# Kernel optimization log

Hardware: AMD Instinct MI355X
Metric: run time of the kernel (lower is better)

Reference implementation:

```python
import jax, jax.numpy as jnp
import numpy as np

SIZE = 8192
DIM = 256
N = 32768
BETA = 0.25
DECAY = 0.99
EPS = 1e-5


def setup_inputs() -> dict:
    key = jax.random.key(0)
    kz, ke = jax.random.split(key)
    z = jax.random.normal(kz, (N, DIM), dtype=jnp.float32)
    # init = randn * 0.1, ema_embed_sum initialized as a clone of embeddings
    embeddings = jax.random.normal(ke, (SIZE, DIM), dtype=jnp.float32) * 0.1
    ema_embed_sum = embeddings
    ema_cluster_size = jnp.zeros((SIZE,), dtype=jnp.float32)
    usage_counter = jnp.zeros((SIZE,), dtype=jnp.int64)
    return {
        "z": z,
        "embeddings": embeddings,
        "ema_cluster_size": ema_cluster_size,
        "ema_embed_sum": ema_embed_sum,
        "usage_counter": usage_counter,
    }


def reference(z, embeddings, ema_cluster_size, ema_embed_sum, usage_counter):
    # Squared euclidean distances; argmin is identical to cdist argmin.
    z2 = jnp.sum(z * z, axis=-1, keepdims=True)              # [N, 1]
    e2 = jnp.sum(embeddings * embeddings, axis=-1)           # [K]
    d2 = z2 - 2.0 * jnp.matmul(z, embeddings.T) + e2         # [N, K]
    indices = jnp.argmin(d2, axis=-1)                         # [N]

    quantized = embeddings[indices]                           # [N, D] gather

    # usage_counter: vectorized equivalent of the per-index python loop
    counts_f = jax.ops.segment_sum(
        jnp.ones((z.shape[0],), dtype=jnp.float32), indices, num_segments=SIZE
    )                                                         # [K] == onehot.sum(0)
    new_usage = usage_counter + counts_f.astype(usage_counter.dtype)

    sg = jax.lax.stop_gradient
    commit_loss = BETA * jnp.mean((z - sg(quantized)) ** 2)
    codebook_loss = jnp.mean((quantized - sg(z)) ** 2)
    loss = commit_loss + codebook_loss

    # EMA update (training mode), all under no-grad semantics
    embed_sum = jax.ops.segment_sum(z, indices, num_segments=SIZE)  # onehot.T @ z
    new_cluster_size = DECAY * ema_cluster_size + (1.0 - DECAY) * counts_f
    new_embed_sum = DECAY * ema_embed_sum + (1.0 - DECAY) * embed_sum
    n = jnp.sum(new_cluster_size)
    cluster = (new_cluster_size + EPS) / (n + SIZE * EPS) * n
    new_embeddings = new_embed_sum / cluster[:, None]

    # straight-through estimator
    quantized_st = z + sg(quantized - z)
    return (indices, quantized_st, loss, new_embeddings, new_cluster_size,
            new_embed_sum, new_usage)
```

## Files before the change

### kernel.cpp

```cpp
#include <hip/hip_runtime.h>

#define NZ 32768
#define KE 8192
#define DD 256
#define NCHUNK 4
#define CH (KE / NCHUNK)
#define NSLICE (NCHUNK * 4)
#define ITERS ((CH / 128) * 8)
#define THR_GAP 0.05f
#define BIASF 128.0f

typedef __attribute__((ext_vector_type(8))) _Float16 f16x8;
typedef __attribute__((ext_vector_type(4))) float f32x4;
typedef unsigned int uint32;


__device__ __forceinline__ float wave_reduce_sum(float v) {
#pragma unroll
  for (int m = 32; m >= 1; m >>= 1) v += __shfl_xor(v, m, 64);
  return v;
}

__global__ void prep_kernel(const float* __restrict__ emb, unsigned short* __restrict__ e_dst,
                            float* __restrict__ e_sq, const float* __restrict__ z,
                            unsigned short* __restrict__ z_dst,
                            const float* __restrict__ ema_cs, float* __restrict__ sema_out,
                            float* __restrict__ o_loss) {
  const int gb = blockIdx.x;
  if (gb < KE / 4) {
    const int row = gb * 4 + (threadIdx.x >> 6);
    const int lane = threadIdx.x & 63;
    const float4 v = *reinterpret_cast<const float4*>(emb + (size_t)row * DD + lane * 4);
    alignas(8) _Float16 hv[4] = {(_Float16)v.x, (_Float16)v.y, (_Float16)v.z, (_Float16)v.w};
    *reinterpret_cast<uint2*>(e_dst + (size_t)row * DD + lane * 4) =
        *reinterpret_cast<const uint2*>(hv);
    float s = (v.x * v.x + v.y * v.y) + (v.z * v.z + v.w * v.w);
    s = wave_reduce_sum(s);
    if (lane == 0) e_sq[row] = s;
  } else if (gb < (KE / 4) + (NZ / 4)) {
    const int row = (gb - KE / 4) * 4 + (threadIdx.x >> 6);
    const int lane = threadIdx.x & 63;
    const float4 v = *reinterpret_cast<const float4*>(z + (size_t)row * DD + lane * 4);
    alignas(8) _Float16 hv[4] = {(_Float16)v.x, (_Float16)v.y, (_Float16)v.z, (_Float16)v.w};
    *reinterpret_cast<uint2*>(z_dst + (size_t)row * DD + lane * 4) =
        *reinterpret_cast<const uint2*>(hv);
  } else {
    __shared__ float red[256];
    float s = 0.f;
    for (int i = threadIdx.x; i < KE; i += 256) s += ema_cs[i];
    red[threadIdx.x] = s;
    __syncthreads();
    for (int off = 128; off >= 1; off >>= 1) {
      if (threadIdx.x < off) red[threadIdx.x] += red[threadIdx.x + off];
      __syncthreads();
    }
    if (threadIdx.x == 0) {
      sema_out[0] = red[0];
      o_loss[0] = 0.f;
    }
  }
}


#define LSTR 32
#define NWIN (ITERS / 4)

#define LDSA(ki, r) (&ldsB[ki][r][0])

#define STAGEB(buf, itv)                                                        \
  {                                                                             \
    const int kb_ = ((itv) & 7) * 32;                                           \
    const size_t bo_ = (size_t)((itv) >> 3) * 128 * DD + kb_;                   \
    __builtin_amdgcn_global_load_lds((const uint32*)(ef + bsw + bo_),           \
                                     (uint32*)&ldsB[buf][wid * 16][0], 16, 0, 0); \
  }

#define STAGEW(SG, ws)                                                          \
  {                                                                             \
    const int s0_ = (ws) * 4;                                                   \
    STAGEB((SG)*4 + 0, s0_ + 0)                                                 \
    STAGEB((SG)*4 + 1, s0_ + 1)                                                 \
    STAGEB((SG)*4 + 2, s0_ + 2)                                                 \
    STAGEB((SG)*4 + 3, s0_ + 3)                                                 \
  }

#define VBAR4                                                  \
  asm volatile("s_waitcnt vmcnt(4)" ::: "memory");             \
  __builtin_amdgcn_s_barrier();                                \
  __builtin_amdgcn_sched_barrier(0);

#define VBAR0                                                  \
  asm volatile("s_waitcnt vmcnt(0)" ::: "memory");             \
  __builtin_amdgcn_s_barrier();                                \
  __builtin_amdgcn_sched_barrier(0);

__launch_bounds__(512, 1)
__global__ void mfma_argmin_kernel(const unsigned short* __restrict__ zf,
                                   const unsigned short* __restrict__ ef,
                                   const float* __restrict__ e2,
                                   float4* __restrict__ pt) {
  __shared__ unsigned short ldsB[16][128][LSTR];
  __shared__ float ldsE2[CH];
  const int bid = blockIdx.x;
  const int c = (bid & 7) >> 1;
  const int mblk = ((bid >> 3) << 1) | (bid & 1);
  const int row0 = mblk * 128;
  const int cbase = c * CH;
  const int tid = threadIdx.x;
  const int wid = tid >> 6, lane = tid & 63;
  const int wr = wid >> 2, wc = wid & 3;
  const int lg = lane >> 4, l15 = lane & 15;

  const int ur = tid >> 2;
  const int usw = (((tid & 3) ^ ((ur >> 1) & 3)) << 3);
  const int csw = ((lg ^ ((l15 >> 1) & 3)) << 3);
  const size_t aoff0 = (size_t)(row0 + ur) * DD + (tid & 3) * 8;
  const size_t bsw = (size_t)(cbase + ur) * DD + ((lane & 3) ^ ((lane >> 3) & 3)) * 8;

  uint32 k1[4][4], k2[4][4];
#pragma unroll
  for (int i = 0; i < 4; ++i)
#pragma unroll
    for (int r = 0; r < 4; ++r) { k1[i][r] = 0u; k2[i][r] = 0u; }

  f32x4 acc[4][2];
  f16x8 areg[8][4];

  for (int i = tid; i < CH; i += 512) ldsE2[i] = BIASF - 0.5f * e2[cbase + i];
#pragma unroll
  for (int ki = 0; ki < 8; ++ki) {
    const uint4 va0 = *reinterpret_cast<const uint4*>(zf + aoff0 + ki * 32);
    *reinterpret_cast<uint4*>(LDSA(ki, ur) + usw) = va0;
  }
  __syncthreads();
#pragma unroll
  for (int ki = 0; ki < 8; ++ki)
#pragma unroll
    for (int x = 0; x < 4; ++x)
      areg[ki][x] =
          *reinterpret_cast<const f16x8*>(LDSA(ki, wr * 64 + x * 16 + l15) + csw);
  __syncthreads();
  STAGEW(0, 0)
  STAGEW(1, 1)
  VBAR4

#define COMPUTE(buf, kil, tl)                                                           \
  {                                                                                     \
    if ((kil) == 0) {                                                                   \
      const int e2o_ = ((tl) << 7) + wc * 32 + l15;                                     \
      const float e0_ = ldsE2[e2o_];                                                    \
      const float e1_ = ldsE2[e2o_ + 16];                                               \
      _Pragma("unroll") for (int i = 0; i < 4; ++i) {                                   \
        acc[i][0] = (f32x4)(e0_);                                                       \
        acc[i][1] = (f32x4)(e1_);                                                       \
      }                                                                                 \
    }                                                                                   \
    f16x8 bh[2];                                                                        \
    _Pragma("unroll") for (int x = 0; x < 2; ++x)                                       \
      bh[x] = *reinterpret_cast<const f16x8*>(&ldsB[buf][wc * 32 + x * 16 + l15][csw]); \
    _Pragma("unroll") for (int i = 0; i < 4; ++i)                                       \
        _Pragma("unroll") for (int j = 0; j < 2; ++j)                                   \
            acc[i][j] = __builtin_amdgcn_mfma_f32_16x16x32_f16(areg[kil][i], bh[j], acc[i][j], 0, 0, 0); \
    if ((kil) == 7) {                                                                   \
      const uint32 tb_ = (uint32)((tl) << 2);                                           \
      _Pragma("unroll") for (int j = 0; j < 2; ++j) {                                   \
        const uint32 meta = tb_ | (uint32)j;                                            \
        _Pragma("unroll") for (int i = 0; i < 4; ++i)                                   \
            _Pragma("unroll") for (int r = 0; r < 4; ++r) {                             \
          const uint32 key = (__float_as_uint(acc[i][j][r]) & 0xFFFFFFC0u) | meta;      \
          const uint32 t = min(k1[i][r], key);                                          \
          k1[i][r] = max(k1[i][r], key);                                                \
          k2[i][r] = max(k2[i][r], t);                                                  \
        }                                                                               \
      }                                                                                 \
    }                                                                                   \
  }

#define WINDOW(G, SG, wv, P)                                                \
  STAGEW(SG, (wv) + 2)                                                      \
  {                                                                         \
    const int tl_ = (wv) >> 1;                                              \
    COMPUTE((G)*4 + 0, (P)*4 + 0, tl_)                                      \
    COMPUTE((G)*4 + 1, (P)*4 + 1, tl_)                                      \
    COMPUTE((G)*4 + 2, (P)*4 + 2, tl_)                                      \
    COMPUTE((G)*4 + 3, (P)*4 + 3, tl_)                                      \
  }                                                                         \
  VBAR4

  for (int W = 0; W < 28; W += 4) {
    WINDOW(0, 2, W + 0, 0)
    WINDOW(1, 3, W + 1, 1)
    WINDOW(2, 0, W + 2, 0)
    WINDOW(3, 1, W + 3, 1)
  }
  WINDOW(0, 2, 28, 0)
  WINDOW(1, 3, 29, 1)
  COMPUTE(8, 0, 15)
  COMPUTE(9, 1, 15)
  COMPUTE(10, 2, 15)
  COMPUTE(11, 3, 15)
  VBAR0
  COMPUTE(12, 4, 15)
  COMPUTE(13, 5, 15)
  COMPUTE(14, 6, 15)
  COMPUTE(15, 7, 15)

  float bv1[4][4], bv2[4][4];
  uint32 bpi[4][4];
  const uint32 cb_ = (uint32)(cbase + wc * 32 + l15);
#pragma unroll
  for (int i = 0; i < 4; ++i)
#pragma unroll
    for (int r = 0; r < 4; ++r) {
      const uint32 a1 = k1[i][r], a2 = k2[i][r];
      bv1[i][r] = 2.f * BIASF - 2.f * __uint_as_float(a1 & 0xFFFFFFC0u);
      bv2[i][r] = 2.f * BIASF - 2.f * __uint_as_float(a2 & 0xFFFFFFC0u);
      const uint32 c1 = cb_ + ((a1 & 60u) >> 2) * 128u + ((a1 & 3u) << 4);
      const uint32 c2 = cb_ + ((a2 & 60u) >> 2) * 128u + ((a2 & 3u) << 4);
      bpi[i][r] = c1 | (c2 << 16);
    }

#pragma unroll
  for (int m = 1; m <= 8; m <<= 1) {
#pragma unroll
    for (int i = 0; i < 4; ++i)
#pragma unroll
      for (int r = 0; r < 4; ++r) {
        const float ov1 = __shfl_xor(bv1[i][r], m, 64);
        const float ov2 = __shfl_xor(bv2[i][r], m, 64);
        const uint32 op = (uint32)__shfl_xor((int)bpi[i][r], m, 64);
        const uint32 ai1 = bpi[i][r] & 0xFFFFu, oi1 = op & 0xFFFFu;
        const bool ol = (ov1 < bv1[i][r]) || (ov1 == bv1[i][r] && oi1 < ai1);
        const float w1 = ol ? ov1 : bv1[i][r];
        const uint32 wi1 = ol ? oi1 : ai1;
        const float w2 = ol ? ov2 : bv2[i][r];
        const uint32 wi2 = ol ? (op >> 16) : (bpi[i][r] >> 16);
        const float l1 = ol ? bv1[i][r] : ov1;
        const uint32 li1 = ol ? ai1 : oi1;
        const bool s2 = (l1 < w2) || (l1 == w2 && li1 < wi2);
        bv1[i][r] = w1;
        bv2[i][r] = s2 ? l1 : w2;
        bpi[i][r] = wi1 | ((s2 ? li1 : wi2) << 16);
      }
  }
  if (l15 == 0) {
    const int slice = c * 4 + wc;
#pragma unroll
    for (int i = 0; i < 4; ++i)
#pragma unroll
      for (int r = 0; r < 4; ++r) {
        const int row = row0 + wr * 64 + i * 16 + lg * 4 + r;
        pt[(size_t)slice * NZ + row] =
            make_float4(bv1[i][r], bv2[i][r], __uint_as_float(bpi[i][r]), 0.f);
      }
  }
}

__global__ void combine_kernel(const float* __restrict__ z, const float* __restrict__ emb,
                               const float* __restrict__ e2,
                               const float4* __restrict__ pt, float* __restrict__ oidx_f,
                               int* __restrict__ oidx_i, float* __restrict__ oq,
                               float* __restrict__ oloss) {
  const int row = blockIdx.x * 4 + (threadIdx.x >> 6);
  const int lane = threadIdx.x & 63;
  const int wid = threadIdx.x >> 6;
  const float4 p = pt[(size_t)(lane & 15) * NZ + row];
  const float v1 = p.x, v2 = p.y;
  const uint32 pk = __float_as_uint(p.z);
  float m = v1;
#pragma unroll
  for (int s = 1; s <= 8; s <<= 1) m = fminf(m, __shfl_xor(m, s, 64));
  const float thr = m + THR_GAP;
  const unsigned long long b1 = __ballot(v1 < thr) & 0xFFFFull;
  const unsigned long long b2 = __ballot(v2 < thr) & 0xFFFFull;

  const float4 zv = *reinterpret_cast<const float4*>(z + (size_t)row * DD + lane * 4);
  float z2r = (zv.x * zv.x + zv.y * zv.y) + (zv.z * zv.z + zv.w * zv.w);
  z2r = wave_reduce_sum(z2r);
  float bestd = 3.4e38f;
  int besti = KE;
  for (unsigned long long mm = b1; mm; mm &= mm - 1) {
    const int l = (int)__builtin_ctzll(mm);
    const uint32 pkc = (uint32)__shfl((int)pk, l, 64);
    const int idxc = (int)(pkc & 0xFFFFu);
    const float4 ev = *reinterpret_cast<const float4*>(emb + (size_t)idxc * DD + lane * 4);
    float s = (zv.x * ev.x + zv.y * ev.y) + (zv.z * ev.z + zv.w * ev.w);
    s = wave_reduce_sum(s);
    const float d = (z2r - 2.f * s) + e2[idxc];
    if (d < bestd || (d == bestd && idxc < besti)) { bestd = d; besti = idxc; }
  }
  for (unsigned long long mm = b2; mm; mm &= mm - 1) {
    const int l = (int)__builtin_ctzll(mm);
    const uint32 pkc = (uint32)__shfl((int)pk, l, 64);
    const int idxc = (int)(pkc >> 16);
    const float4 ev = *reinterpret_cast<const float4*>(emb + (size_t)idxc * DD + lane * 4);
    float s = (zv.x * ev.x + zv.y * ev.y) + (zv.z * ev.z + zv.w * ev.w);
    s = wave_reduce_sum(s);
    const float d = (z2r - 2.f * s) + e2[idxc];
    if (d < bestd || (d == bestd && idxc < besti)) { bestd = d; besti = idxc; }
  }
  if (lane == 0) {
    oidx_f[row] = (float)besti;
    oidx_i[row] = besti;
  }
  const float4 qv = *reinterpret_cast<const float4*>(emb + (size_t)besti * DD + lane * 4);
  *reinterpret_cast<float4*>(oq + (size_t)row * DD + lane * 4) = qv;
  const float dx = zv.x - qv.x, dy = zv.y - qv.y, dz = zv.z - qv.z, dw = zv.w - qv.w;
  float s = (dx * dx + dy * dy) + (dz * dz + dw * dw);
  s = wave_reduce_sum(s);
  __shared__ float red[4];
  if (lane == 0) red[wid] = s;
  __syncthreads();
  if (threadIdx.x == 0) {
    const float t = (red[0] + red[1]) + (red[2] + red[3]);
    atomicAdd(oloss, t * (1.25f / ((float)NZ * (float)DD)));
  }
}

__global__ void perk_kernel(const float* __restrict__ z, const float* __restrict__ ema_cs,
                            const float* __restrict__ ema_es, const int* __restrict__ usage,
                            const int* __restrict__ idx, const float* __restrict__ sema,
                            float* __restrict__ o_emb, float* __restrict__ o_cs,
                            float* __restrict__ o_es, float* __restrict__ o_us) {
  const int k0 = blockIdx.x * 8;
  const int tid = threadIdx.x;
  __shared__ int cnt;
  __shared__ int cnt8[8];
  __shared__ int stot[8];
  __shared__ int rows[2048];
  float acc[8];
#pragma unroll
  for (int q = 0; q < 8; ++q) acc[q] = 0.f;
  if (tid < 8) stot[tid] = 0;
  for (int base = 0; base < NZ; base += 2048) {
    if (tid == 0) cnt = 0;
    if (tid < 8) cnt8[tid] = 0;
    __syncthreads();
#pragma unroll
    for (int t = 0; t < 2048; t += 256) {
      const int r = base + t + tid;
      const int q = idx[r] - k0;
      if ((unsigned)q < 8u) {
        rows[atomicAdd(&cnt, 1)] = (r << 3) | q;
        atomicAdd(&cnt8[q], 1);
      }
    }
    __syncthreads();
    const int cq = cnt;
    if (tid < 8) stot[tid] += cnt8[tid];
    for (int m = 0; m < cq; ++m) {
      const int rr = rows[m];
      const float v = z[(size_t)(rr >> 3) * DD + tid];
      const int q = rr & 7;
#pragma unroll
      for (int qq = 0; qq < 8; ++qq)
        if (qq == q) acc[qq] += v;
    }
    __syncthreads();
  }
  const float n = 0.99f * sema[0] + 0.01f * (float)NZ;
  const float dn = n + (float)KE * 1e-5f;
#pragma unroll
  for (int q = 0; q < 8; ++q) {
    const float ncs = 0.99f * ema_cs[k0 + q] + 0.01f * (float)stot[q];
    const float nes = 0.99f * ema_es[(size_t)(k0 + q) * DD + tid] + 0.01f * acc[q];
    o_es[(size_t)(k0 + q) * DD + tid] = nes;
    o_emb[(size_t)(k0 + q) * DD + tid] = nes / ((ncs + 1e-5f) / dn * n);
  }
  if (tid < 8) {
    o_cs[k0 + tid] = 0.99f * ema_cs[k0 + tid] + 0.01f * (float)stot[tid];
    o_us[k0 + tid] = (float)(usage[k0 + tid] + stot[tid]);
  }
}


extern "C" void kernel_launch(void* const* d_in, const int* in_sizes, int n_in,
                              void* d_out, int out_size, void* d_ws, size_t ws_size,
                              hipStream_t stream) {
  const float* z = (const float*)d_in[0];
  const float* emb = (const float*)d_in[1];
  const float* ema_cs = (const float*)d_in[2];
  const float* ema_es = (const float*)d_in[3];
  const int* usage = (const int*)d_in[4];

  float* out = (float*)d_out;
  float* o_idx = out;
  float* o_q = o_idx + NZ;
  float* o_loss = o_q + (size_t)NZ * DD;
  float* o_emb = o_loss + 1;
  float* o_cs = o_emb + (size_t)KE * DD;
  float* o_es = o_cs + KE;
  float* o_us = o_es + (size_t)KE * DD;

  char* w = (char*)d_ws;
  size_t off = 0;
  auto alloc = [&](size_t bytes) -> char* {
    char* r = w + off;
    off = (off + bytes + 255) & ~(size_t)255;
    return r;
  };
  float* ws_e2 = (float*)alloc(KE * 4);
  float* ws_sema = (float*)alloc(256);
  int* ws_idx = (int*)alloc(NZ * 4);
  float4* ws_pt = (float4*)alloc((size_t)NSLICE * NZ * 16);
  unsigned short* z_f16 = (unsigned short*)alloc((size_t)NZ * DD * 2);
  unsigned short* e_f16 = (unsigned short*)alloc((size_t)KE * DD * 2);
  (void)ws_size;

  prep_kernel<<<(KE / 4) + (NZ / 4) + 1, 256, 0, stream>>>(emb, e_f16, ws_e2, z, z_f16,
                                                           ema_cs, ws_sema, o_loss);

  mfma_argmin_kernel<<<(NZ / 128) * NCHUNK, 512, 0, stream>>>(z_f16, e_f16, ws_e2, ws_pt);
  combine_kernel<<<NZ / 4, 256, 0, stream>>>(z, emb, ws_e2, ws_pt, o_idx, ws_idx,
                                             o_q, o_loss);
  perk_kernel<<<KE / 8, 256, 0, stream>>>(z, ema_cs, ema_es, usage, ws_idx, ws_sema,
                                          o_emb, o_cs, o_es, o_us);
}
```

Measured before the change: 340.6 us.

## Switch argmin GEMM from 16x16x32 to 32x32x16 MFMA tiles

Rewrites the distance-GEMM inner loop to use 32x32x16 f16 MFMA instructions with 16-element accumulators instead of 16x16x32 tiles, and remaps the A/B register fragments, LDS swizzled reads, top-2 key tracking, cross-lane reduction and output row mapping to match. Larger MFMA tiles give more math per LDS fragment load and fewer instructions issued per K step. The cost is a longer cross-lane shuffle reduction (5 rounds over 32 lanes), more accumulator and key registers per thread, and a more intricate row-index mapping that has to be exactly right.

```diff
diff --git a/kernel.cpp b/kernel.cpp
--- a/kernel.cpp
+++ b/kernel.cpp
@@ -12,6 +12,7 @@
 
 typedef __attribute__((ext_vector_type(8))) _Float16 f16x8;
 typedef __attribute__((ext_vector_type(4))) float f32x4;
+typedef __attribute__((ext_vector_type(16))) float f32x16;
 typedef unsigned int uint32;
 
 
@@ -109,22 +110,22 @@
   const int tid = threadIdx.x;
   const int wid = tid >> 6, lane = tid & 63;
   const int wr = wid >> 2, wc = wid & 3;
-  const int lg = lane >> 4, l15 = lane & 15;
+  const int l31 = lane & 31, lh = lane >> 5;
+  const int swq = (l31 >> 1) & 3;
 
   const int ur = tid >> 2;
   const int usw = (((tid & 3) ^ ((ur >> 1) & 3)) << 3);
-  const int csw = ((lg ^ ((l15 >> 1) & 3)) << 3);
   const size_t aoff0 = (size_t)(row0 + ur) * DD + (tid & 3) * 8;
   const size_t bsw = (size_t)(cbase + ur) * DD + ((lane & 3) ^ ((lane >> 3) & 3)) * 8;
 
-  uint32 k1[4][4], k2[4][4];
-#pragma unroll
-  for (int i = 0; i < 4; ++i)
-#pragma unroll
-    for (int r = 0; r < 4; ++r) { k1[i][r] = 0u; k2[i][r] = 0u; }
-
-  f32x4 acc[4][2];
-  f16x8 areg[8][4];
+  uint32 k1[2][16], k2[2][16];
+#pragma unroll
+  for (int T = 0; T < 2; ++T)
+#pragma unroll
+    for (int r = 0; r < 16; ++r) { k1[T][r] = 0u; k2[T][r] = 0u; }
+
+  f32x16 acc[2];
+  f16x8 areg[16][2];
 
   for (int i = tid; i < CH; i += 512) ldsE2[i] = BIASF - 0.5f * e2[cbase + i];
 #pragma unroll
@@ -134,11 +135,11 @@
   }
   __syncthreads();
 #pragma unroll
-  for (int ki = 0; ki < 8; ++ki)
-#pragma unroll
-    for (int x = 0; x < 4; ++x)
-      areg[ki][x] =
-          *reinterpret_cast<const f16x8*>(LDSA(ki, wr * 64 + x * 16 + l15) + csw);
+  for (int s = 0; s < 16; ++s)
+#pragma unroll
+    for (int T = 0; T < 2; ++T)
+      areg[s][T] = *reinterpret_cast<const f16x8*>(
+          LDSA(s >> 1, wr * 64 + T * 32 + l31) + ((((s & 1) * 2 + lh) ^ swq) << 3));
   __syncthreads();
   STAGEW(0, 0)
   STAGEW(1, 1)
@@ -147,32 +148,27 @@
 #define COMPUTE(buf, kil, tl)                                                           \
   {                                                                                     \
     if ((kil) == 0) {                                                                   \
-      const int e2o_ = ((tl) << 7) + wc * 32 + l15;                                     \
-      const float e0_ = ldsE2[e2o_];                                                    \
-      const float e1_ = ldsE2[e2o_ + 16];                                               \
-      _Pragma("unroll") for (int i = 0; i < 4; ++i) {                                   \
-        acc[i][0] = (f32x4)(e0_);                                                       \
-        acc[i][1] = (f32x4)(e1_);                                                       \
-      }                                                                                 \
+      const float e_ = ldsE2[((tl) << 7) + wc * 32 + l31];                              \
+      acc[0] = (f32x16)(e_);                                                            \
+      acc[1] = (f32x16)(e_);                                                            \
     }                                                                                   \
     f16x8 bh[2];                                                                        \
-    _Pragma("unroll") for (int x = 0; x < 2; ++x)                                       \
-      bh[x] = *reinterpret_cast<const f16x8*>(&ldsB[buf][wc * 32 + x * 16 + l15][csw]); \
-    _Pragma("unroll") for (int i = 0; i < 4; ++i)                                       \
-        _Pragma("unroll") for (int j = 0; j < 2; ++j)                                   \
-            acc[i][j] = __builtin_amdgcn_mfma_f32_16x16x32_f16(areg[kil][i], bh[j], acc[i][j], 0, 0, 0); \
+    _Pragma("unroll") for (int h = 0; h < 2; ++h)                                       \
+      bh[h] = *reinterpret_cast<const f16x8*>(                                          \
+          &ldsB[buf][wc * 32 + l31][((h * 2 + lh) ^ swq) << 3]);                        \
+    _Pragma("unroll") for (int h = 0; h < 2; ++h)                                       \
+      _Pragma("unroll") for (int T = 0; T < 2; ++T)                                     \
+        acc[T] = __builtin_amdgcn_mfma_f32_32x32x16_f16(areg[(kil) * 2 + h][T], bh[h],  \
+                                                        acc[T], 0, 0, 0);               \
     if ((kil) == 7) {                                                                   \
-      const uint32 tb_ = (uint32)((tl) << 2);                                           \
-      _Pragma("unroll") for (int j = 0; j < 2; ++j) {                                   \
-        const uint32 meta = tb_ | (uint32)j;                                            \
-        _Pragma("unroll") for (int i = 0; i < 4; ++i)                                   \
-            _Pragma("unroll") for (int r = 0; r < 4; ++r) {                             \
-          const uint32 key = (__float_as_uint(acc[i][j][r]) & 0xFFFFFFC0u) | meta;      \
-          const uint32 t = min(k1[i][r], key);                                          \
-          k1[i][r] = max(k1[i][r], key);                                                \
-          k2[i][r] = max(k2[i][r], t);                                                  \
+      const uint32 meta = (uint32)((tl) << 2);                                          \
+      _Pragma("unroll") for (int T = 0; T < 2; ++T)                                     \
+        _Pragma("unroll") for (int r = 0; r < 16; ++r) {                                \
+          const uint32 key = (__float_as_uint(acc[T][r]) & 0xFFFFFFC0u) | meta;         \
+          const uint32 t = min(k1[T][r], key);                                          \
+          k1[T][r] = max(k1[T][r], key);                                                \
+          k2[T][r] = max(k2[T][r], t);                                                  \
         }                                                                               \
-      }                                                                                 \
     }                                                                                   \
   }
 
@@ -205,53 +201,53 @@
   COMPUTE(14, 6, 15)
   COMPUTE(15, 7, 15)
 
-  float bv1[4][4], bv2[4][4];
-  uint32 bpi[4][4];
-  const uint32 cb_ = (uint32)(cbase + wc * 32 + l15);
-#pragma unroll
-  for (int i = 0; i < 4; ++i)
-#pragma unroll
-    for (int r = 0; r < 4; ++r) {
-      const uint32 a1 = k1[i][r], a2 = k2[i][r];
-      bv1[i][r] = 2.f * BIASF - 2.f * __uint_as_float(a1 & 0xFFFFFFC0u);
-      bv2[i][r] = 2.f * BIASF - 2.f * __uint_as_float(a2 & 0xFFFFFFC0u);
-      const uint32 c1 = cb_ + ((a1 & 60u) >> 2) * 128u + ((a1 & 3u) << 4);
-      const uint32 c2 = cb_ + ((a2 & 60u) >> 2) * 128u + ((a2 & 3u) << 4);
-      bpi[i][r] = c1 | (c2 << 16);
+  float bv1[2][16], bv2[2][16];
+  uint32 bpi[2][16];
+  const uint32 cb_ = (uint32)(cbase + wc * 32 + l31);
+#pragma unroll
+  for (int T = 0; T < 2; ++T)
+#pragma unroll
+    for (int r = 0; r < 16; ++r) {
+      const uint32 a1 = k1[T][r], a2 = k2[T][r];
+      bv1[T][r] = 2.f * BIASF - 2.f * __uint_as_float(a1 & 0xFFFFFFC0u);
+      bv2[T][r] = 2.f * BIASF - 2.f * __uint_as_float(a2 & 0xFFFFFFC0u);
+      const uint32 c1 = cb_ + ((a1 & 60u) >> 2) * 128u;
+      const uint32 c2 = cb_ + ((a2 & 60u) >> 2) * 128u;
+      bpi[T][r] = c1 | (c2 << 16);
     }
 
 #pragma unroll
-  for (int m = 1; m <= 8; m <<= 1) {
-#pragma unroll
-    for (int i = 0; i < 4; ++i)
-#pragma unroll
-      for (int r = 0; r < 4; ++r) {
-        const float ov1 = __shfl_xor(bv1[i][r], m, 64);
-        const float ov2 = __shfl_xor(bv2[i][r], m, 64);
-        const uint32 op = (uint32)__shfl_xor((int)bpi[i][r], m, 64);
-        const uint32 ai1 = bpi[i][r] & 0xFFFFu, oi1 = op & 0xFFFFu;
-        const bool ol = (ov1 < bv1[i][r]) || (ov1 == bv1[i][r] && oi1 < ai1);
-        const float w1 = ol ? ov1 : bv1[i][r];
+  for (int m = 1; m <= 16; m <<= 1) {
+#pragma unroll
+    for (int T = 0; T < 2; ++T)
+#pragma unroll
+      for (int r = 0; r < 16; ++r) {
+        const float ov1 = __shfl_xor(bv1[T][r], m, 64);
+        const float ov2 = __shfl_xor(bv2[T][r], m, 64);
+        const uint32 op = (uint32)__shfl_xor((int)bpi[T][r], m, 64);
+        const uint32 ai1 = bpi[T][r] & 0xFFFFu, oi1 = op & 0xFFFFu;
+        const bool ol = (ov1 < bv1[T][r]) || (ov1 == bv1[T][r] && oi1 < ai1);
+        const float w1 = ol ? ov1 : bv1[T][r];
         const uint32 wi1 = ol ? oi1 : ai1;
-        const float w2 = ol ? ov2 : bv2[i][r];
-        const uint32 wi2 = ol ? (op >> 16) : (bpi[i][r] >> 16);
-        const float l1 = ol ? bv1[i][r] : ov1;
+        const float w2 = ol ? ov2 : bv2[T][r];
+        const uint32 wi2 = ol ? (op >> 16) : (bpi[T][r] >> 16);
+        const float l1 = ol ? bv1[T][r] : ov1;
         const uint32 li1 = ol ? ai1 : oi1;
         const bool s2 = (l1 < w2) || (l1 == w2 && li1 < wi2);
-        bv1[i][r] = w1;
-        bv2[i][r] = s2 ? l1 : w2;
-        bpi[i][r] = wi1 | ((s2 ? li1 : wi2) << 16);
+        bv1[T][r] = w1;
+        bv2[T][r] = s2 ? l1 : w2;
+        bpi[T][r] = wi1 | ((s2 ? li1 : wi2) << 16);
       }
   }
-  if (l15 == 0) {
+  if (l31 == 0) {
     const int slice = c * 4 + wc;
 #pragma unroll
-    for (int i = 0; i < 4; ++i)
-#pragma unroll
-      for (int r = 0; r < 4; ++r) {
-        const int row = row0 + wr * 64 + i * 16 + lg * 4 + r;
+    for (int T = 0; T < 2; ++T)
+#pragma unroll
+      for (int r = 0; r < 16; ++r) {
+        const int row = row0 + wr * 64 + T * 32 + (r & 3) + 8 * (r >> 2) + 4 * lh;
         pt[(size_t)slice * NZ + row] =
-            make_float4(bv1[i][r], bv2[i][r], __uint_as_float(bpi[i][r]), 0.f);
+            make_float4(bv1[T][r], bv2[T][r], __uint_as_float(bpi[T][r]), 0.f);
       }
   }
 }
```

Measured after the change: 956.0 us. 181% more time.
